# Kernel optimization log

Hardware: AMD Instinct MI355X
Metric: run time of the kernel (lower is better)

## Reference

```python
import jax, jax.numpy as jnp
import numpy as np

CHANNELS = 64
WEIGHT_NUMS = [66 * 64, 64 * 64, 64]  # layer0 (C+2)->C, layer1 C->C, layer2 C->1
BIAS_NUMS = [64, 64, 1]
NUM_GEN_PARAMS = sum(WEIGHT_NUMS) + sum(BIAS_NUMS)  # 8513


def setup_inputs() -> dict:
    key = jax.random.key(0)
    k1, k2 = jax.random.split(key)
    N, C, H, W = 4, 64, 80, 200
    num_ins = 8  # instances per image -> M = 32 total
    M = N * num_ins
    x = jax.random.normal(k1, (N, C, H, W), dtype=jnp.float32)
    mask_head_params = jax.random.normal(k2, (M, NUM_GEN_PARAMS), dtype=jnp.float32) * 0.1
    return {"x": x, "mask_head_params": mask_head_params, "num_ins": num_ins}


def reference(x, mask_head_params, num_ins):
    N, C, H, W = x.shape
    ch = CHANNELS
    # compute_locations with stride=1 (stride//2 == 0); source bug divides the
    # whole tensor by W (locations[:1,:,:] /= W on a batch-1 tensor).
    xx, yy = jnp.meshgrid(jnp.arange(W, dtype=x.dtype), jnp.arange(H, dtype=x.dtype), indexing='xy')
    loc = jnp.stack([xx, yy], axis=0) / W  # [2, H, W]
    xa = jnp.concatenate([jnp.broadcast_to(loc[None], (N, 2, H, W)), x], axis=1)  # [N, C+2, H, W]
    feats = jnp.repeat(xa, num_ins, axis=0)  # [M, C+2, H, W] per-instance inputs
    M = feats.shape[0]
    # parse_dynamic_params: split generated params into per-layer weights/biases
    splits = np.cumsum(WEIGHT_NUMS + BIAS_NUMS)[:-1]
    w0, w1, w2, b0, b1, b2 = jnp.split(mask_head_params, splits, axis=1)
    w0 = w0.reshape(M, ch, ch + 2)
    w1 = w1.reshape(M, ch, ch)
    w2 = w2.reshape(M, 1, ch)
    b2 = b2 - 2.19  # mask bias shift (is_mask=True)
    # grouped 1x1 convs (groups=M) as per-instance GEMMs with ReLU between layers
    h = jax.nn.relu(jnp.einsum('mkc,mchw->mkhw', w0, feats) + b0[:, :, None, None])
    h = jax.nn.relu(jnp.einsum('mkc,mchw->mkhw', w1, h) + b1[:, :, None, None])
    out = jnp.einsum('mkc,mchw->mkhw', w2, h) + b2[:, :, None, None]
    return out.reshape(1, -1, H, W)  # [1, M*out_channels, H, W]
```

## Files before the change

kernel.cpp:

```cpp
#include <hip/hip_runtime.h>

typedef __attribute__((ext_vector_type(8))) short    short8;
typedef __attribute__((ext_vector_type(4))) float    f32x4;
typedef __attribute__((ext_vector_type(4))) unsigned uint4_;
typedef __attribute__((ext_vector_type(2))) unsigned uint2_;

#define HW     16000
#define WWID   200
#define NPARAM 8513
#define PACK_STRIDE 6144

__device__ __forceinline__ unsigned f2bf(float f) {
    unsigned u = __builtin_bit_cast(unsigned, f);
    return (u + 0x7FFFu + ((u >> 16) & 1u)) >> 16;
}
__device__ __forceinline__ unsigned pkbf2(float a, float b) {
    return f2bf(a) | (f2bf(b) << 16);
}

__device__ __forceinline__ float w0val(const float* pm, int k, int c) {
    if (c < 64)  return pm[k * 66 + c + 2];
    if (c == 64) return pm[k * 66 + 0];
    if (c == 65) return pm[k * 66 + 1];
    if (c == 66) return pm[8384 + k];
    return 0.0f;
}

__global__ __launch_bounds__(256) void pack_weights(
    const float* __restrict__ params, unsigned* __restrict__ wp)
{
    const int m   = blockIdx.x;
    const int tid = threadIdx.x;
    const float* pm = params + (size_t)m * NPARAM;
    unsigned* dst = wp + (size_t)m * PACK_STRIDE;

    const int l  = tid >> 2;
    const int i0 = (tid & 3) * 2;
    #pragma unroll
    for (int frag = 0; frag < 12; ++frag) {
        int ch = frag >> 2, kb = frag & 3;
        int k = kb * 16 + (l & 15);
        int c = ch * 32 + (l >> 4) * 8 + i0;
        dst[frag * 256 + tid] = pkbf2(w0val(pm, k, c), w0val(pm, k, c + 1));
    }
    #pragma unroll
    for (int frag = 0; frag < 8; ++frag) {
        int ch = frag >> 2, kb = frag & 3;
        int k = kb * 16 + (l & 15);
        int c = ch * 32 + (l >> 4) * 8 + i0;
        const float* s = pm + 4224 + k * 64 + c;
        dst[3072 + frag * 256 + tid] = pkbf2(s[0], s[1]);
    }
    float* fd = (float*)dst;
    if (tid < 64) {
        fd[5120 + tid] = pm[8448 + tid];
        fd[5184 + tid] = pm[8320 + tid];
    }
    if (tid == 0) fd[5248] = pm[8512];
}

__global__ __launch_bounds__(512) void condlane_mfma2(
    const float* __restrict__ x,
    const unsigned* __restrict__ wp,
    float* __restrict__ out,
    int num_ins)
{
    extern __shared__ char lds[];
    char* xt = lds;
    const int tid  = threadIdx.x;
    const int lane = tid & 63;
    const int wid  = tid >> 6;
    const int n    = blockIdx.y;
    const int pxg0 = blockIdx.x * 256;
    char* h0 = lds + 65536 + wid * 2048;

    {
        const int p   = tid & 255;
        const int sel = tid >> 8;
        const int pc  = min(pxg0 + p, HW - 1);
        const float* xp = x + (size_t)n * 64 * HW + pc;
        #pragma unroll
        for (int it = 0; it < 4; ++it) {
            int c0 = sel * 32 + it * 8;
            uint4_ d;
            d.x = pkbf2(xp[(size_t)(c0 + 0) * HW], xp[(size_t)(c0 + 1) * HW]);
            d.y = pkbf2(xp[(size_t)(c0 + 2) * HW], xp[(size_t)(c0 + 3) * HW]);
            d.z = pkbf2(xp[(size_t)(c0 + 4) * HW], xp[(size_t)(c0 + 5) * HW]);
            d.w = pkbf2(xp[(size_t)(c0 + 6) * HW], xp[(size_t)(c0 + 7) * HW]);
            int byte = (p * 256 + c0 * 2) ^ ((p & 15) << 4);
            *(uint4_*)(xt + byte) = d;
        }
        const int pg = pxg0 + p;
        float lx = (float)(pg % WWID) * (1.0f / WWID);
        float ly = (float)(pg / WWID) * (1.0f / WWID);
        uint4_ z; z.x = 0; z.y = 0; z.z = 0; z.w = 0;
        uint4_ cv; cv.x = pkbf2(lx, ly); cv.y = pkbf2(1.0f, 0.0f); cv.z = 0; cv.w = 0;
        int ba = (p * 256 + 128 + sel * 32) ^ ((p & 15) << 4);
        int bb = (p * 256 + 144 + sel * 32) ^ ((p & 15) << 4);
        *(uint4_*)(xt + ba) = (sel == 0) ? cv : z;
        *(uint4_*)(xt + bb) = z;
    }
    __syncthreads();

    if (wid >= num_ins) return;
    const int m = n * num_ins + wid;
    const unsigned* wm = wp + (size_t)m * PACK_STRIDE;
    const int g  = (lane >> 4) & 3;
    const int hi = lane >> 4;

    short8 w0f[3][4], w1f[2][4];
    #pragma unroll
    for (int ch = 0; ch < 3; ++ch)
        #pragma unroll
        for (int kb = 0; kb < 4; ++kb)
            w0f[ch][kb] = *(const short8*)(wm + (ch * 4 + kb) * 256 + lane * 4);
    #pragma unroll
    for (int ch = 0; ch < 2; ++ch)
        #pragma unroll
        for (int kb = 0; kb < 4; ++kb)
            w1f[ch][kb] = *(const short8*)(wm + 3072 + (ch * 4 + kb) * 256 + lane * 4);
    const float* sm = (const float*)wm;
    f32x4 bias1[4], w2v[4];
    #pragma unroll
    for (int kb = 0; kb < 4; ++kb) {
        bias1[kb] = *(const f32x4*)(sm + 5120 + kb * 16 + g * 4);
        w2v[kb]   = *(const f32x4*)(sm + 5184 + kb * 16 + g * 4);
    }
    const float b2 = sm[5248] - 2.19f;

    const int nsl = min(16, (HW - pxg0) >> 4);
    const int hpx = lane & 15;

    for (int s = 0; s < nsl; ++s) {
        const int pxl = s * 16 + (lane & 15);
        short8 xf[3];
        #pragma unroll
        for (int ch = 0; ch < 3; ++ch) {
            int byte = (pxl * 256 + ch * 64 + hi * 16) ^ ((pxl & 15) << 4);
            xf[ch] = *(const short8*)(xt + byte);
        }
        f32x4 acc0[4];
        #pragma unroll
        for (int kb = 0; kb < 4; ++kb) { acc0[kb][0] = 0.f; acc0[kb][1] = 0.f; acc0[kb][2] = 0.f; acc0[kb][3] = 0.f; }
        #pragma unroll
        for (int ch = 0; ch < 3; ++ch)
            #pragma unroll
            for (int kb = 0; kb < 4; ++kb)
                acc0[kb] = __builtin_amdgcn_mfma_f32_16x16x32_bf16(w0f[ch][kb], xf[ch], acc0[kb], 0, 0, 0);
        #pragma unroll
        for (int kb = 0; kb < 4; ++kb) {
            uint2_ pk;
            pk.x = pkbf2(fmaxf(acc0[kb][0], 0.f), fmaxf(acc0[kb][1], 0.f));
            pk.y = pkbf2(fmaxf(acc0[kb][2], 0.f), fmaxf(acc0[kb][3], 0.f));
            int byte = (hpx * 128 + kb * 32 + g * 8) ^ ((hpx & 7) << 4);
            *(uint2_*)(h0 + byte) = pk;
        }
        short8 hf[2];
        #pragma unroll
        for (int ch = 0; ch < 2; ++ch) {
            int byte = (hpx * 128 + ch * 64 + hi * 16) ^ ((hpx & 7) << 4);
            hf[ch] = *(const short8*)(h0 + byte);
        }
        f32x4 acc1[4];
        #pragma unroll
        for (int kb = 0; kb < 4; ++kb) acc1[kb] = bias1[kb];
        #pragma unroll
        for (int ch = 0; ch < 2; ++ch)
            #pragma unroll
            for (int kb = 0; kb < 4; ++kb)
                acc1[kb] = __builtin_amdgcn_mfma_f32_16x16x32_bf16(w1f[ch][kb], hf[ch], acc1[kb], 0, 0, 0);
        float v = 0.f;
        #pragma unroll
        for (int kb = 0; kb < 4; ++kb)
            #pragma unroll
            for (int j = 0; j < 4; ++j)
                v += w2v[kb][j] * fmaxf(acc1[kb][j], 0.f);
        v += __shfl_xor(v, 16);
        v += __shfl_xor(v, 32);
        if (lane < 16)
            out[(size_t)m * HW + pxg0 + s * 16 + lane] = v + b2;
    }
}

extern "C" void kernel_launch(void* const* d_in, const int* in_sizes, int n_in,
                              void* d_out, int out_size, void* d_ws, size_t ws_size,
                              hipStream_t stream) {
    const float* x      = (const float*)d_in[0];
    const float* params = (const float*)d_in[1];
    float* out          = (float*)d_out;

    const int N = in_sizes[0] / (64 * HW);
    const int M = in_sizes[1] / NPARAM;
    const int num_ins = M / N;

    pack_weights<<<M, 256, 0, stream>>>(params, (unsigned*)d_ws);

    dim3 grid((HW + 255) / 256, N);
    condlane_mfma2<<<grid, 512, 81920, stream>>>(x, (const unsigned*)d_ws, out, num_ins);
}
```

Baseline: 27.56 us.

## Fuse weight packing into the main kernel and interleave two pixel slices

Drops the separate pack_weights launch. Each wave now reads its instance's fp32 parameters straight from global memory and converts them to bf16 MFMA fragments in registers, before the barrier, so the loads overlap with staging x into LDS. The main loop processes two 16-pixel slices per iteration, each with its own h0 LDS scratch, to expose more independent MFMA work. In exchange it raises register pressure and LDS use, issues more redundant strided global reads per block, and drops the guard for waves beyond num_ins.

```diff
diff --git a/kernel.cpp b/kernel.cpp
--- a/kernel.cpp
+++ b/kernel.cpp
@@ -8,7 +8,6 @@
 #define HW     16000
 #define WWID   200
 #define NPARAM 8513
-#define PACK_STRIDE 6144
 
 __device__ __forceinline__ unsigned f2bf(float f) {
     unsigned u = __builtin_bit_cast(unsigned, f);
@@ -17,51 +16,14 @@
 __device__ __forceinline__ unsigned pkbf2(float a, float b) {
     return f2bf(a) | (f2bf(b) << 16);
 }
-
-__device__ __forceinline__ float w0val(const float* pm, int k, int c) {
-    if (c < 64)  return pm[k * 66 + c + 2];
-    if (c == 64) return pm[k * 66 + 0];
-    if (c == 65) return pm[k * 66 + 1];
-    if (c == 66) return pm[8384 + k];
-    return 0.0f;
+__device__ __forceinline__ short8 mk8(unsigned a, unsigned b, unsigned c, unsigned d) {
+    uint4_ u; u.x = a; u.y = b; u.z = c; u.w = d;
+    return __builtin_bit_cast(short8, u);
 }
 
-__global__ __launch_bounds__(256) void pack_weights(
-    const float* __restrict__ params, unsigned* __restrict__ wp)
-{
-    const int m   = blockIdx.x;
-    const int tid = threadIdx.x;
-    const float* pm = params + (size_t)m * NPARAM;
-    unsigned* dst = wp + (size_t)m * PACK_STRIDE;
-
-    const int l  = tid >> 2;
-    const int i0 = (tid & 3) * 2;
-    #pragma unroll
-    for (int frag = 0; frag < 12; ++frag) {
-        int ch = frag >> 2, kb = frag & 3;
-        int k = kb * 16 + (l & 15);
-        int c = ch * 32 + (l >> 4) * 8 + i0;
-        dst[frag * 256 + tid] = pkbf2(w0val(pm, k, c), w0val(pm, k, c + 1));
-    }
-    #pragma unroll
-    for (int frag = 0; frag < 8; ++frag) {
-        int ch = frag >> 2, kb = frag & 3;
-        int k = kb * 16 + (l & 15);
-        int c = ch * 32 + (l >> 4) * 8 + i0;
-        const float* s = pm + 4224 + k * 64 + c;
-        dst[3072 + frag * 256 + tid] = pkbf2(s[0], s[1]);
-    }
-    float* fd = (float*)dst;
-    if (tid < 64) {
-        fd[5120 + tid] = pm[8448 + tid];
-        fd[5184 + tid] = pm[8320 + tid];
-    }
-    if (tid == 0) fd[5248] = pm[8512];
-}
-
-__global__ __launch_bounds__(512) void condlane_mfma2(
+__global__ __launch_bounds__(512, 1) void condlane_fused(
     const float* __restrict__ x,
-    const unsigned* __restrict__ wp,
+    const float* __restrict__ params,
     float* __restrict__ out,
     int num_ins)
 {
@@ -72,7 +34,8 @@
     const int wid  = tid >> 6;
     const int n    = blockIdx.y;
     const int pxg0 = blockIdx.x * 256;
-    char* h0 = lds + 65536 + wid * 2048;
+    char* h0a = lds + 65536 + wid * 4096;
+    char* h0b = h0a + 2048;
 
     {
         const int p   = tid & 255;
@@ -100,85 +63,115 @@
         *(uint4_*)(xt + ba) = (sel == 0) ? cv : z;
         *(uint4_*)(xt + bb) = z;
     }
-    __syncthreads();
 
-    if (wid >= num_ins) return;
-    const int m = n * num_ins + wid;
-    const unsigned* wm = wp + (size_t)m * PACK_STRIDE;
+    const int m  = n * num_ins + wid;
     const int g  = (lane >> 4) & 3;
     const int hi = lane >> 4;
+    const float* pm = params + (size_t)m * NPARAM;
 
     short8 w0f[3][4], w1f[2][4];
     #pragma unroll
-    for (int ch = 0; ch < 3; ++ch)
+    for (int kb = 0; kb < 4; ++kb) {
+        const int k = kb * 16 + (lane & 15);
         #pragma unroll
-        for (int kb = 0; kb < 4; ++kb)
-            w0f[ch][kb] = *(const short8*)(wm + (ch * 4 + kb) * 256 + lane * 4);
-    #pragma unroll
-    for (int ch = 0; ch < 2; ++ch)
+        for (int ch = 0; ch < 2; ++ch) {
+            const float* s = pm + k * 66 + 2 + ch * 32 + hi * 8;
+            w0f[ch][kb] = mk8(pkbf2(s[0], s[1]), pkbf2(s[2], s[3]),
+                              pkbf2(s[4], s[5]), pkbf2(s[6], s[7]));
+        }
+        {
+            float a = (hi == 0) ? pm[k * 66 + 0] : 0.0f;
+            float b = (hi == 0) ? pm[k * 66 + 1] : 0.0f;
+            float c = (hi == 0) ? pm[8384 + k]   : 0.0f;
+            w0f[2][kb] = mk8(pkbf2(a, b), pkbf2(c, 0.0f), 0u, 0u);
+        }
         #pragma unroll
-        for (int kb = 0; kb < 4; ++kb)
-            w1f[ch][kb] = *(const short8*)(wm + 3072 + (ch * 4 + kb) * 256 + lane * 4);
-    const float* sm = (const float*)wm;
+        for (int ch = 0; ch < 2; ++ch) {
+            const float* s = pm + 4224 + k * 64 + ch * 32 + hi * 8;
+            w1f[ch][kb] = mk8(pkbf2(s[0], s[1]), pkbf2(s[2], s[3]),
+                              pkbf2(s[4], s[5]), pkbf2(s[6], s[7]));
+        }
+    }
     f32x4 bias1[4], w2v[4];
     #pragma unroll
-    for (int kb = 0; kb < 4; ++kb) {
-        bias1[kb] = *(const f32x4*)(sm + 5120 + kb * 16 + g * 4);
-        w2v[kb]   = *(const f32x4*)(sm + 5184 + kb * 16 + g * 4);
-    }
-    const float b2 = sm[5248] - 2.19f;
+    for (int kb = 0; kb < 4; ++kb)
+        #pragma unroll
+        for (int j = 0; j < 4; ++j) {
+            bias1[kb][j] = pm[8448 + kb * 16 + g * 4 + j];
+            w2v[kb][j]   = pm[8320 + kb * 16 + g * 4 + j];
+        }
+    const float b2 = pm[8512] - 2.19f;
+
+    __syncthreads();
 
     const int nsl = min(16, (HW - pxg0) >> 4);
     const int hpx = lane & 15;
+    const int swz = (lane & 15) << 4;
 
-    for (int s = 0; s < nsl; ++s) {
-        const int pxl = s * 16 + (lane & 15);
-        short8 xf[3];
+    for (int sA = 0; sA < 8; ++sA) {
+        const int sB = sA + 8;
+        const int pxlA = sA * 16 + hpx;
+        const int pxlB = pxlA + 128;
+        short8 xfA[3], xfB[3];
         #pragma unroll
         for (int ch = 0; ch < 3; ++ch) {
-            int byte = (pxl * 256 + ch * 64 + hi * 16) ^ ((pxl & 15) << 4);
-            xf[ch] = *(const short8*)(xt + byte);
+            xfA[ch] = *(const short8*)(xt + ((pxlA * 256 + ch * 64 + hi * 16) ^ swz));
+            xfB[ch] = *(const short8*)(xt + ((pxlB * 256 + ch * 64 + hi * 16) ^ swz));
         }
-        f32x4 acc0[4];
+        f32x4 acc0A[4], acc0B[4];
         #pragma unroll
-        for (int kb = 0; kb < 4; ++kb) { acc0[kb][0] = 0.f; acc0[kb][1] = 0.f; acc0[kb][2] = 0.f; acc0[kb][3] = 0.f; }
+        for (int kb = 0; kb < 4; ++kb)
+            #pragma unroll
+            for (int j = 0; j < 4; ++j) { acc0A[kb][j] = 0.f; acc0B[kb][j] = 0.f; }
         #pragma unroll
         for (int ch = 0; ch < 3; ++ch)
             #pragma unroll
-            for (int kb = 0; kb < 4; ++kb)
-                acc0[kb] = __builtin_amdgcn_mfma_f32_16x16x32_bf16(w0f[ch][kb], xf[ch], acc0[kb], 0, 0, 0);
+            for (int kb = 0; kb < 4; ++kb) {
+                acc0A[kb] = __builtin_amdgcn_mfma_f32_16x16x32_bf16(w0f[ch][kb], xfA[ch], acc0A[kb], 0, 0, 0);
+                acc0B[kb] = __builtin_amdgcn_mfma_f32_16x16x32_bf16(w0f[ch][kb], xfB[ch], acc0B[kb], 0, 0, 0);
+            }
         #pragma unroll
         for (int kb = 0; kb < 4; ++kb) {
-            uint2_ pk;
-            pk.x = pkbf2(fmaxf(acc0[kb][0], 0.f), fmaxf(acc0[kb][1], 0.f));
-            pk.y = pkbf2(fmaxf(acc0[kb][2], 0.f), fmaxf(acc0[kb][3], 0.f));
+            uint2_ pkA, pkB;
+            pkA.x = pkbf2(fmaxf(acc0A[kb][0], 0.f), fmaxf(acc0A[kb][1], 0.f));
+            pkA.y = pkbf2(fmaxf(acc0A[kb][2], 0.f), fmaxf(acc0A[kb][3], 0.f));
+            pkB.x = pkbf2(fmaxf(acc0B[kb][0], 0.f), fmaxf(acc0B[kb][1], 0.f));
+            pkB.y = pkbf2(fmaxf(acc0B[kb][2], 0.f), fmaxf(acc0B[kb][3], 0.f));
             int byte = (hpx * 128 + kb * 32 + g * 8) ^ ((hpx & 7) << 4);
-            *(uint2_*)(h0 + byte) = pk;
+            *(uint2_*)(h0a + byte) = pkA;
+            *(uint2_*)(h0b + byte) = pkB;
         }
-        short8 hf[2];
+        short8 hfA[2], hfB[2];
         #pragma unroll
         for (int ch = 0; ch < 2; ++ch) {
             int byte = (hpx * 128 + ch * 64 + hi * 16) ^ ((hpx & 7) << 4);
-            hf[ch] = *(const short8*)(h0 + byte);
+            hfA[ch] = *(const short8*)(h0a + byte);
+            hfB[ch] = *(const short8*)(h0b + byte);
         }
-        f32x4 acc1[4];
+        f32x4 acc1A[4], acc1B[4];
         #pragma unroll
-        for (int kb = 0; kb < 4; ++kb) acc1[kb] = bias1[kb];
+        for (int kb = 0; kb < 4; ++kb) { acc1A[kb] = bias1[kb]; acc1B[kb] = bias1[kb]; }
         #pragma unroll
         for (int ch = 0; ch < 2; ++ch)
             #pragma unroll
-            for (int kb = 0; kb < 4; ++kb)
-                acc1[kb] = __builtin_amdgcn_mfma_f32_16x16x32_bf16(w1f[ch][kb], hf[ch], acc1[kb], 0, 0, 0);
-        float v = 0.f;
+            for (int kb = 0; kb < 4; ++kb) {
+                acc1A[kb] = __builtin_amdgcn_mfma_f32_16x16x32_bf16(w1f[ch][kb], hfA[ch], acc1A[kb], 0, 0, 0);
+                acc1B[kb] = __builtin_amdgcn_mfma_f32_16x16x32_bf16(w1f[ch][kb], hfB[ch], acc1B[kb], 0, 0, 0);
+            }
+        float vA = 0.f, vB = 0.f;
         #pragma unroll
         for (int kb = 0; kb < 4; ++kb)
             #pragma unroll
-            for (int j = 0; j < 4; ++j)
-                v += w2v[kb][j] * fmaxf(acc1[kb][j], 0.f);
-        v += __shfl_xor(v, 16);
-        v += __shfl_xor(v, 32);
+            for (int j = 0; j < 4; ++j) {
+                vA += w2v[kb][j] * fmaxf(acc1A[kb][j], 0.f);
+                vB += w2v[kb][j] * fmaxf(acc1B[kb][j], 0.f);
+            }
+        vA += __shfl_xor(vA, 16); vA += __shfl_xor(vA, 32);
+        vB += __shfl_xor(vB, 16); vB += __shfl_xor(vB, 32);
         if (lane < 16)
-            out[(size_t)m * HW + pxg0 + s * 16 + lane] = v + b2;
+            out[(size_t)m * HW + pxg0 + sA * 16 + lane] = vA + b2;
+        else if (lane < 32 && sB < nsl)
+            out[(size_t)m * HW + pxg0 + sB * 16 + (lane - 16)] = vB + b2;
     }
 }
 
@@ -193,8 +186,6 @@
     const int M = in_sizes[1] / NPARAM;
     const int num_ins = M / N;
 
-    pack_weights<<<M, 256, 0, stream>>>(params, (unsigned*)d_ws);
-
     dim3 grid((HW + 255) / 256, N);
-    condlane_mfma2<<<grid, 512, 81920, stream>>>(x, (const unsigned*)d_ws, out, num_ins);
+    condlane_fused<<<grid, 512, 98304, stream>>>(x, params, out, num_ins);
 }
```

Result: faster. 26.30 us (-4.6%).

## Drop weight-pack kernel, keep hidden activations in registers via 16x16x16 MFMA

Applied to the files above, without the earlier changes.

Removes the separate pack_weights launch: each wave now loads and converts its instance's weights straight from the fp32 params into MFMA fragments, overlapping this with the x tile staging. The layer-0 accumulator layout is reused directly as the B operand of 16x16x16 bf16 MFMAs for layer 1, so the LDS round-trip for hidden activations goes away and LDS drops to 64 KB. This allows two blocks per CU, and conversion now uses the hardware v_cvt_pk_bf16_f32 instruction. In exchange, the weight loads are strided and uncoalesced and are repeated by every block, the kernel relies on inline asm with hand-placed s_nops for MFMA hazards, and the early exit for waves with wid >= num_ins is removed.

```diff
diff --git a/kernel.cpp b/kernel.cpp
--- a/kernel.cpp
+++ b/kernel.cpp
@@ -1,78 +1,48 @@
 #include <hip/hip_runtime.h>
 
-typedef __attribute__((ext_vector_type(8))) short    short8;
-typedef __attribute__((ext_vector_type(4))) float    f32x4;
-typedef __attribute__((ext_vector_type(4))) unsigned uint4_;
-typedef __attribute__((ext_vector_type(2))) unsigned uint2_;
+typedef __attribute__((ext_vector_type(8)))  short    short8;
+typedef __attribute__((ext_vector_type(4)))  short    s16x4;
+typedef __attribute__((ext_vector_type(4)))  float    f32x4;
+typedef __attribute__((ext_vector_type(4)))  unsigned uint4_;
+typedef __attribute__((ext_vector_type(2)))  unsigned uint2_;
 
 #define HW     16000
 #define WWID   200
 #define NPARAM 8513
-#define PACK_STRIDE 6144
 
-__device__ __forceinline__ unsigned f2bf(float f) {
-    unsigned u = __builtin_bit_cast(unsigned, f);
-    return (u + 0x7FFFu + ((u >> 16) & 1u)) >> 16;
+__device__ __forceinline__ unsigned pkbf2(float a, float b) {
+    unsigned r;
+    asm("v_cvt_pk_bf16_f32 %0, %1, %2" : "=v"(r) : "v"(a), "v"(b));
+    return r;
 }
-__device__ __forceinline__ unsigned pkbf2(float a, float b) {
-    return f2bf(a) | (f2bf(b) << 16);
+__device__ __forceinline__ short8 mk8(unsigned a, unsigned b, unsigned c, unsigned d) {
+    uint4_ u; u.x = a; u.y = b; u.z = c; u.w = d;
+    return __builtin_bit_cast(short8, u);
+}
+__device__ __forceinline__ s16x4 mk4(unsigned a, unsigned b) {
+    uint2_ u; u.x = a; u.y = b;
+    return __builtin_bit_cast(s16x4, u);
+}
+__device__ __forceinline__ void mfma16(f32x4& acc, s16x4 a, s16x4 b) {
+    asm("s_nop 2\n\tv_mfma_f32_16x16x16_bf16 %0, %1, %2, %0"
+        : "+v"(acc) : "v"(a), "v"(b));
 }
 
-__device__ __forceinline__ float w0val(const float* pm, int k, int c) {
-    if (c < 64)  return pm[k * 66 + c + 2];
-    if (c == 64) return pm[k * 66 + 0];
-    if (c == 65) return pm[k * 66 + 1];
-    if (c == 66) return pm[8384 + k];
-    return 0.0f;
-}
-
-__global__ __launch_bounds__(256) void pack_weights(
-    const float* __restrict__ params, unsigned* __restrict__ wp)
-{
-    const int m   = blockIdx.x;
-    const int tid = threadIdx.x;
-    const float* pm = params + (size_t)m * NPARAM;
-    unsigned* dst = wp + (size_t)m * PACK_STRIDE;
-
-    const int l  = tid >> 2;
-    const int i0 = (tid & 3) * 2;
-    #pragma unroll
-    for (int frag = 0; frag < 12; ++frag) {
-        int ch = frag >> 2, kb = frag & 3;
-        int k = kb * 16 + (l & 15);
-        int c = ch * 32 + (l >> 4) * 8 + i0;
-        dst[frag * 256 + tid] = pkbf2(w0val(pm, k, c), w0val(pm, k, c + 1));
-    }
-    #pragma unroll
-    for (int frag = 0; frag < 8; ++frag) {
-        int ch = frag >> 2, kb = frag & 3;
-        int k = kb * 16 + (l & 15);
-        int c = ch * 32 + (l >> 4) * 8 + i0;
-        const float* s = pm + 4224 + k * 64 + c;
-        dst[3072 + frag * 256 + tid] = pkbf2(s[0], s[1]);
-    }
-    float* fd = (float*)dst;
-    if (tid < 64) {
-        fd[5120 + tid] = pm[8448 + tid];
-        fd[5184 + tid] = pm[8320 + tid];
-    }
-    if (tid == 0) fd[5248] = pm[8512];
-}
-
-__global__ __launch_bounds__(512) void condlane_mfma2(
+__global__ __launch_bounds__(512, 2) void condlane_reg(
     const float* __restrict__ x,
-    const unsigned* __restrict__ wp,
+    const float* __restrict__ params,
     float* __restrict__ out,
     int num_ins)
 {
-    extern __shared__ char lds[];
-    char* xt = lds;
+    extern __shared__ char lds_[];
+    char* xt = lds_;
     const int tid  = threadIdx.x;
     const int lane = tid & 63;
     const int wid  = tid >> 6;
     const int n    = blockIdx.y;
     const int pxg0 = blockIdx.x * 256;
-    char* h0 = lds + 65536 + wid * 2048;
+    const int g    = (lane >> 4) & 3;
+    const int px16 = lane & 15;
 
     {
         const int p   = tid & 255;
@@ -87,97 +57,98 @@
             d.y = pkbf2(xp[(size_t)(c0 + 2) * HW], xp[(size_t)(c0 + 3) * HW]);
             d.z = pkbf2(xp[(size_t)(c0 + 4) * HW], xp[(size_t)(c0 + 5) * HW]);
             d.w = pkbf2(xp[(size_t)(c0 + 6) * HW], xp[(size_t)(c0 + 7) * HW]);
-            int byte = (p * 256 + c0 * 2) ^ ((p & 15) << 4);
-            *(uint4_*)(xt + byte) = d;
+            *(uint4_*)(xt + ((p * 256 + c0 * 2) ^ ((p & 15) << 4))) = d;
         }
         const int pg = pxg0 + p;
         float lx = (float)(pg % WWID) * (1.0f / WWID);
         float ly = (float)(pg / WWID) * (1.0f / WWID);
-        uint4_ z; z.x = 0; z.y = 0; z.z = 0; z.w = 0;
-        uint4_ cv; cv.x = pkbf2(lx, ly); cv.y = pkbf2(1.0f, 0.0f); cv.z = 0; cv.w = 0;
+        uint4_ z;  z.x = 0; z.y = 0; z.z = 0; z.w = 0;
+        uint4_ cv; cv.x = pkbf2(lx, ly); cv.y = pkbf2(1.f, 0.f); cv.z = 0; cv.w = 0;
         int ba = (p * 256 + 128 + sel * 32) ^ ((p & 15) << 4);
         int bb = (p * 256 + 144 + sel * 32) ^ ((p & 15) << 4);
         *(uint4_*)(xt + ba) = (sel == 0) ? cv : z;
         *(uint4_*)(xt + bb) = z;
     }
+
+    const int m = n * num_ins + wid;
+    const float* pm = params + (size_t)m * NPARAM;
+
+    short8 w0f[3][4];
+    s16x4  w1f4[4][4];
+    #pragma unroll
+    for (int kb = 0; kb < 4; ++kb) {
+        const int k = kb * 16 + px16;
+        #pragma unroll
+        for (int ch = 0; ch < 2; ++ch) {
+            const float* s0 = pm + k * 66 + 2 + ch * 32 + g * 8;
+            w0f[ch][kb] = mk8(pkbf2(s0[0], s0[1]), pkbf2(s0[2], s0[3]),
+                              pkbf2(s0[4], s0[5]), pkbf2(s0[6], s0[7]));
+        }
+        float a = (g == 0) ? pm[k * 66 + 0] : 0.f;
+        float b = (g == 0) ? pm[k * 66 + 1] : 0.f;
+        float c = (g == 0) ? pm[8384 + k]   : 0.f;
+        w0f[2][kb] = mk8(pkbf2(a, b), pkbf2(c, 0.f), 0u, 0u);
+        #pragma unroll
+        for (int ks = 0; ks < 4; ++ks) {
+            const float* s1 = pm + 4224 + (kb * 16 + px16) * 64 + ks * 16 + g * 4;
+            w1f4[kb][ks] = mk4(pkbf2(s1[0], s1[1]), pkbf2(s1[2], s1[3]));
+        }
+    }
+    f32x4 bias1[4], w2v[4];
+    #pragma unroll
+    for (int kb = 0; kb < 4; ++kb)
+        #pragma unroll
+        for (int r = 0; r < 4; ++r) {
+            bias1[kb][r] = pm[8448 + kb * 16 + g * 4 + r];
+            w2v[kb][r]   = pm[8320 + kb * 16 + g * 4 + r];
+        }
+    const float b2 = pm[8512] - 2.19f;
+
     __syncthreads();
 
-    if (wid >= num_ins) return;
-    const int m = n * num_ins + wid;
-    const unsigned* wm = wp + (size_t)m * PACK_STRIDE;
-    const int g  = (lane >> 4) & 3;
-    const int hi = lane >> 4;
+    const int swz = px16 << 4;
+    const int nsl = min(16, (HW - pxg0) >> 4);
 
-    short8 w0f[3][4], w1f[2][4];
-    #pragma unroll
-    for (int ch = 0; ch < 3; ++ch)
+    for (int s = 0; s < 16; ++s) {
+        const int pxl = s * 16 + px16;
+        short8 xf[3];
+        #pragma unroll
+        for (int ch = 0; ch < 3; ++ch)
+            xf[ch] = *(const short8*)(xt + ((pxl * 256 + ch * 64 + g * 16) ^ swz));
+        f32x4 acc0[4];
         #pragma unroll
         for (int kb = 0; kb < 4; ++kb)
-            w0f[ch][kb] = *(const short8*)(wm + (ch * 4 + kb) * 256 + lane * 4);
-    #pragma unroll
-    for (int ch = 0; ch < 2; ++ch)
-        #pragma unroll
-        for (int kb = 0; kb < 4; ++kb)
-            w1f[ch][kb] = *(const short8*)(wm + 3072 + (ch * 4 + kb) * 256 + lane * 4);
-    const float* sm = (const float*)wm;
-    f32x4 bias1[4], w2v[4];
-    #pragma unroll
-    for (int kb = 0; kb < 4; ++kb) {
-        bias1[kb] = *(const f32x4*)(sm + 5120 + kb * 16 + g * 4);
-        w2v[kb]   = *(const f32x4*)(sm + 5184 + kb * 16 + g * 4);
-    }
-    const float b2 = sm[5248] - 2.19f;
-
-    const int nsl = min(16, (HW - pxg0) >> 4);
-    const int hpx = lane & 15;
-
-    for (int s = 0; s < nsl; ++s) {
-        const int pxl = s * 16 + (lane & 15);
-        short8 xf[3];
-        #pragma unroll
-        for (int ch = 0; ch < 3; ++ch) {
-            int byte = (pxl * 256 + ch * 64 + hi * 16) ^ ((pxl & 15) << 4);
-            xf[ch] = *(const short8*)(xt + byte);
-        }
-        f32x4 acc0[4];
-        #pragma unroll
-        for (int kb = 0; kb < 4; ++kb) { acc0[kb][0] = 0.f; acc0[kb][1] = 0.f; acc0[kb][2] = 0.f; acc0[kb][3] = 0.f; }
+            #pragma unroll
+            for (int j = 0; j < 4; ++j) acc0[kb][j] = 0.f;
         #pragma unroll
         for (int ch = 0; ch < 3; ++ch)
             #pragma unroll
             for (int kb = 0; kb < 4; ++kb)
                 acc0[kb] = __builtin_amdgcn_mfma_f32_16x16x32_bf16(w0f[ch][kb], xf[ch], acc0[kb], 0, 0, 0);
+        s16x4 hf[4];
         #pragma unroll
-        for (int kb = 0; kb < 4; ++kb) {
-            uint2_ pk;
-            pk.x = pkbf2(fmaxf(acc0[kb][0], 0.f), fmaxf(acc0[kb][1], 0.f));
-            pk.y = pkbf2(fmaxf(acc0[kb][2], 0.f), fmaxf(acc0[kb][3], 0.f));
-            int byte = (hpx * 128 + kb * 32 + g * 8) ^ ((hpx & 7) << 4);
-            *(uint2_*)(h0 + byte) = pk;
-        }
-        short8 hf[2];
-        #pragma unroll
-        for (int ch = 0; ch < 2; ++ch) {
-            int byte = (hpx * 128 + ch * 64 + hi * 16) ^ ((hpx & 7) << 4);
-            hf[ch] = *(const short8*)(h0 + byte);
-        }
+        for (int ks = 0; ks < 4; ++ks)
+            hf[ks] = mk4(pkbf2(fmaxf(acc0[ks][0], 0.f), fmaxf(acc0[ks][1], 0.f)),
+                         pkbf2(fmaxf(acc0[ks][2], 0.f), fmaxf(acc0[ks][3], 0.f)));
         f32x4 acc1[4];
         #pragma unroll
         for (int kb = 0; kb < 4; ++kb) acc1[kb] = bias1[kb];
         #pragma unroll
-        for (int ch = 0; ch < 2; ++ch)
+        for (int ks = 0; ks < 4; ++ks)
             #pragma unroll
             for (int kb = 0; kb < 4; ++kb)
-                acc1[kb] = __builtin_amdgcn_mfma_f32_16x16x32_bf16(w1f[ch][kb], hf[ch], acc1[kb], 0, 0, 0);
+                mfma16(acc1[kb], w1f4[kb][ks], hf[ks]);
+        asm("s_nop 7\n\ts_nop 7"
+            : "+v"(acc1[0]), "+v"(acc1[1]), "+v"(acc1[2]), "+v"(acc1[3]));
         float v = 0.f;
         #pragma unroll
         for (int kb = 0; kb < 4; ++kb)
             #pragma unroll
-            for (int j = 0; j < 4; ++j)
-                v += w2v[kb][j] * fmaxf(acc1[kb][j], 0.f);
+            for (int r = 0; r < 4; ++r)
+                v += w2v[kb][r] * fmaxf(acc1[kb][r], 0.f);
         v += __shfl_xor(v, 16);
         v += __shfl_xor(v, 32);
-        if (lane < 16)
+        if (lane < 16 && s < nsl)
             out[(size_t)m * HW + pxg0 + s * 16 + lane] = v + b2;
     }
 }
@@ -193,8 +164,6 @@
     const int M = in_sizes[1] / NPARAM;
     const int num_ins = M / N;
 
-    pack_weights<<<M, 256, 0, stream>>>(params, (unsigned*)d_ws);
-
     dim3 grid((HW + 255) / 256, N);
-    condlane_mfma2<<<grid, 512, 81920, stream>>>(x, (const unsigned*)d_ws, out, num_ins);
+    condlane_reg<<<grid, 512, 65536, stream>>>(x, params, out, num_ins);
 }
```

Result: faster. 26.25 us, median of 2 (-4.7%).
